# Kernel tuning notes

Measured on AMD Instinct MI355X. Metric: run time of the kernel, lower is better.

## Reference

```python
import jax, jax.numpy as jnp
import numpy as np

N_REC = 12288  # 12 * nside^2, nside=32


def _mlp(x, w1, b1, w2, b2):
    # two-layer MLP with SiLU, as in GraphCast-style edge embedders
    return jnp.dot(jax.nn.silu(jnp.dot(x, w1) + b1), w2) + b2


def setup_inputs() -> dict:
    key = jax.random.key(0)
    ks = jax.random.split(key, 12)
    B, E, D_X, D_EDGE = 2, 393216, 128, 4
    EDGE_IN, EDGE_OUT, LIN_OUT = D_EDGE + D_X, 256, 256

    def glorot(k, shape):
        fan = shape[0] + shape[1]
        return jax.random.normal(k, shape, jnp.float32) * jnp.sqrt(2.0 / fan)

    return {
        "x": jax.random.normal(ks[0], (B, E, D_X), jnp.float32),
        "edge_attr": jax.random.normal(ks[1], (E, D_EDGE), jnp.float32),
        "edge_index": jax.random.randint(ks[2], (2, E), 0, N_REC, jnp.int64),
        "w1e": glorot(ks[3], (EDGE_IN, EDGE_OUT)),
        "b1e": jnp.zeros((EDGE_OUT,), jnp.float32),
        "w2e": glorot(ks[4], (EDGE_OUT, EDGE_OUT)),
        "b2e": jnp.zeros((EDGE_OUT,), jnp.float32),
        "w1f": glorot(ks[5], (EDGE_OUT, LIN_OUT)),
        "b1f": jnp.zeros((LIN_OUT,), jnp.float32),
        "w2f": glorot(ks[6], (LIN_OUT, LIN_OUT)),
        "b2f": jnp.zeros((LIN_OUT,), jnp.float32),
    }


def reference(x, edge_attr, edge_index, w1e, b1e, w2e, b2e, w1f, b1f, w2f, b2f):
    B = x.shape[0]
    # broadcast edge_attr over batch and concat with per-edge grid features
    ea = jnp.broadcast_to(edge_attr[None], (B,) + edge_attr.shape)  # [B,E,d_edge]
    v_g_prime = jnp.concatenate([ea, x], axis=-1)                    # [B,E,edge_in]
    v_g = _mlp(v_g_prime, w1e, b1e, w2e, b2e)                        # [B,E,edge_out]
    # scatter-sum edges into receiver nodes (edge_index[1]) along dim 1
    recv = edge_index[1]
    v_m_sum = jnp.zeros((B, N_REC, v_g.shape[-1]), v_g.dtype).at[:, recv].add(v_g)
    return _mlp(v_m_sum, w1f, b1f, w2f, b2f)                         # [B,N_REC,lin_out]
```

## Files before the change

### kernel.cpp

```cpp
#include <hip/hip_runtime.h>
#include <hip/hip_bf16.h>

#define E_EDGES 393216
#define NRECV   12288
#define DX      128
#define BATCH   2

typedef short bf16x8 __attribute__((ext_vector_type(8)));
typedef float f32x4  __attribute__((ext_vector_type(4)));

__device__ __forceinline__ unsigned short f2bf(float f) {
  union { float f; unsigned u; } v; v.f = f;
  unsigned r = v.u + 0x7FFFu + ((v.u >> 16) & 1u);
  return (unsigned short)(r >> 16);
}

__device__ __forceinline__ unsigned pk2(float a, float b) {
  __hip_bfloat162 h = __float22bfloat162_rn(make_float2(a, b));
  union { __hip_bfloat162 h; unsigned u; } c; c.h = h;
  return c.u;
}

__device__ __forceinline__ float silu_f(float v) {
  return v / (1.0f + __expf(-v));
}

__global__ __launch_bounds__(256) void zero_kernel(float4* __restrict__ p, int n4) {
  int i = blockIdx.x * 256 + threadIdx.x;
  int stride = gridDim.x * 256;
  float4 z = make_float4(0.f, 0.f, 0.f, 0.f);
  for (; i < n4; i += stride) p[i] = z;
}

__global__ void swz_kernel(const float* __restrict__ W,
                           unsigned short* __restrict__ out, int K, int N) {
  int t = blockIdx.x * 256 + threadIdx.x;
  if (t >= K * N) return;
  int j = t & 7;
  int l = (t >> 3) & 63;
  int rest = t >> 9;
  int nfr = N >> 4;
  int nf = rest % nfr;
  int ks = rest / nfr;
  int k = ks * 32 + (l >> 4) * 8 + j;
  int n = nf * 16 + (l & 15);
  out[t] = f2bf(W[k * N + n]);
}

__global__ void swz_w1e_kernel(const float* __restrict__ W, const float* __restrict__ bias,
                               unsigned short* __restrict__ out) {
  int t = blockIdx.x * 256 + threadIdx.x;
  int j = t & 7;
  int l = (t >> 3) & 63;
  int rest = t >> 9;
  int nf = rest & 15;
  int ks = rest >> 4;
  int k = ks * 32 + (l >> 4) * 8 + j;
  int n = nf * 16 + (l & 15);
  float v = (k < 132) ? W[k * 256 + n] : (k == 132 ? bias[n] : 0.0f);
  out[t] = f2bf(v);
}

__global__ void hist_kernel(const int* __restrict__ recv, int* __restrict__ cnt) {
  int e = blockIdx.x * 256 + threadIdx.x;
  if (e < E_EDGES) atomicAdd(&cnt[recv[e]], 1);
}

__global__ __launch_bounds__(256) void scan_kernel(const int* __restrict__ cnt,
                                                   int* __restrict__ head) {
  __shared__ int ts[256];
  const int t = threadIdx.x;
  const int base = t * 48;
  int s = 0;
#pragma unroll
  for (int i = 0; i < 48; ++i) s += cnt[base + i];
  ts[t] = s;
  __syncthreads();
  for (int d = 1; d < 256; d <<= 1) {
    int v = (t >= d) ? ts[t - d] : 0;
    __syncthreads();
    ts[t] += v;
    __syncthreads();
  }
  int run = (t == 0) ? 0 : ts[t - 1];
  for (int i = 0; i < 48; ++i) { head[base + i] = run; run += cnt[base + i]; }
}

__global__ void scatter_kernel(const int* __restrict__ recv, int* __restrict__ head,
                               int* __restrict__ perm) {
  int e = blockIdx.x * 256 + threadIdx.x;
  if (e < E_EDGES) {
    int pos = atomicAdd(&head[recv[e]], 1);
    perm[pos] = e;
  }
}

__global__ __launch_bounds__(256, 4) void edge_kernel(
    const float* __restrict__ x, const float* __restrict__ edge_attr,
    const int* __restrict__ recv, const int* __restrict__ perm,
    const unsigned short* __restrict__ w1sw, float* __restrict__ s) {
  __shared__ __align__(16) char hsT[256 * 144];
  __shared__ __align__(16) char indT[16 * 144];
  __shared__ unsigned int seg32[16];
  __shared__ int seg_recv[64];
  __shared__ int ev[64];
  __shared__ int rs[64];
  char* As = hsT;

  const int tid = threadIdx.x;
  const int l  = tid & 63;
  const int w  = tid >> 6;
  const int lo = l & 15, hi = l >> 4;
  const int p0 = blockIdx.x * 64;
  const int b  = blockIdx.y;

  if (tid < 64) {
    int e = perm[p0 + tid];
    ev[tid] = e;
    rs[tid] = recv[e];
  }
  for (int idx = tid; idx < 960; idx += 256) {
    int r = idx / 15, k2 = idx - r * 15;
    int byte0 = 264 + 8 * k2;
    uint2 vz = make_uint2(k2 == 0 ? 0x00003F80u : 0u, 0u);
    *(uint2*)(As + r * 384 + (byte0 ^ ((r & 7) << 4))) = vz;
  }
  __syncthreads();

  {
    const int r = tid >> 2, q = tid & 3;
    const int e = ev[r];
    const int rx = (r & 7) << 4;
    const float4* xr = (const float4*)(x + ((size_t)b * E_EDGES + e) * DX);
#pragma unroll
    for (int i = 0; i < 8; ++i) {
      int t = i * 4 + q;
      float4 v = xr[t];
      int byte0 = 8 + 8 * t;
      *(uint2*)(As + r * 384 + (byte0 ^ rx)) = make_uint2(pk2(v.x, v.y), pk2(v.z, v.w));
    }
  }
  const int flag = (l == 63) || (rs[l + 1] != rs[l]);
  const unsigned long long segmask = __ballot(flag);
  const int nseg = __popcll(segmask);
  if (tid < 64) {
    float4 ea = *(const float4*)(edge_attr + (size_t)ev[tid] * 4);
    *(uint2*)(As + tid * 384 + ((tid & 7) << 4)) =
        make_uint2(pk2(ea.x, ea.y), pk2(ea.z, ea.w));
    int sid = __popcll(segmask & ((1ull << tid) - 1ull));
    ((unsigned char*)seg32)[tid] = (unsigned char)sid;
    if (flag) seg_recv[sid] = rs[tid];
  }
  __syncthreads();

  {
    int m = tid & 15, k4 = tid >> 4;
    unsigned four = seg32[k4];
    unsigned um = (unsigned)m;
    unsigned e0 = ((four & 255u) == um) ? 0x3F80u : 0u;
    unsigned e1 = (((four >> 8) & 255u) == um) ? 0x3F80u : 0u;
    unsigned e2 = (((four >> 16) & 255u) == um) ? 0x3F80u : 0u;
    unsigned e3 = ((four >> 24) == um) ? 0x3F80u : 0u;
    *(uint2*)(indT + m * 144 + k4 * 8) = make_uint2(e0 | (e1 << 16), e2 | (e3 << 16));
  }

  f32x4 acc[4][4] = {};
  const int axor = (lo & 7) << 4;
#pragma unroll
  for (int kk = 0; kk < 5; ++kk) {
    bf16x8 a[4], bb[4];
#pragma unroll
    for (int mf = 0; mf < 4; ++mf)
      a[mf] = *(const bf16x8*)(As + (mf * 16 + lo) * 384 + ((kk * 64 + hi * 16) ^ axor));
#pragma unroll
    for (int nf = 0; nf < 4; ++nf)
      bb[nf] = *(const bf16x8*)&w1sw[(size_t)(((kk * 16) + (w * 4 + nf)) * 64 + l) * 8];
#pragma unroll
    for (int mf = 0; mf < 4; ++mf)
#pragma unroll
      for (int nf = 0; nf < 4; ++nf)
        acc[mf][nf] = __builtin_amdgcn_mfma_f32_16x16x32_bf16(a[mf], bb[nf], acc[mf][nf], 0, 0, 0);
  }
  __syncthreads();

#pragma unroll
  for (int mf = 0; mf < 4; ++mf) {
#pragma unroll
    for (int nf = 0; nf < 4; ++nf) {
      const int col = w * 64 + nf * 16 + lo;
      float v0 = silu_f(acc[mf][nf][0]);
      float v1 = silu_f(acc[mf][nf][1]);
      float v2 = silu_f(acc[mf][nf][2]);
      float v3 = silu_f(acc[mf][nf][3]);
      *(uint2*)(hsT + col * 144 + (mf * 16 + hi * 4) * 2) =
          make_uint2(pk2(v0, v1), pk2(v2, v3));
    }
  }
  __syncthreads();

  float* sb = s + (size_t)b * NRECV * 256;
  for (int p = 0;;) {
    f32x4 accS[4] = {};
#pragma unroll
    for (int kk = 0; kk < 2; ++kk) {
      bf16x8 a = *(const bf16x8*)(indT + lo * 144 + kk * 64 + hi * 16);
#pragma unroll
      for (int nf = 0; nf < 4; ++nf) {
        bf16x8 bb = *(const bf16x8*)(hsT + (w * 64 + nf * 16 + lo) * 144 + kk * 64 + hi * 16);
        accS[nf] = __builtin_amdgcn_mfma_f32_16x16x32_bf16(a, bb, accS[nf], 0, 0, 0);
      }
    }
#pragma unroll
    for (int j = 0; j < 4; ++j) {
      int sidx = p * 16 + hi * 4 + j;
      if (sidx < nseg) {
        int rcv = seg_recv[sidx];
#pragma unroll
        for (int nf = 0; nf < 4; ++nf)
          atomicAdd(sb + (size_t)rcv * 256 + w * 64 + nf * 16 + lo, accS[nf][j]);
      }
    }
    ++p;
    if (p * 16 >= nseg) break;
    __syncthreads();
    {
      int m = tid & 15, k4 = tid >> 4;
      unsigned four = seg32[k4];
      unsigned um = (unsigned)(m + p * 16);
      unsigned e0 = ((four & 255u) == um) ? 0x3F80u : 0u;
      unsigned e1 = (((four >> 8) & 255u) == um) ? 0x3F80u : 0u;
      unsigned e2 = (((four >> 16) & 255u) == um) ? 0x3F80u : 0u;
      unsigned e3 = ((four >> 24) == um) ? 0x3F80u : 0u;
      *(uint2*)(indT + m * 144 + k4 * 8) = make_uint2(e0 | (e1 << 16), e2 | (e3 << 16));
    }
    __syncthreads();
  }
}

__device__ __forceinline__ void gemm64(const unsigned short* Ns,
                                       const unsigned short* __restrict__ Bsw,
                                       int w, int l, f32x4 acc[4][4]) {
  const int lo = l & 15, hi = l >> 4;
#pragma unroll
  for (int kk = 0; kk < 8; ++kk) {
    bf16x8 a[4], bb[4];
#pragma unroll
    for (int mf = 0; mf < 4; ++mf)
      a[mf] = *(const bf16x8*)&Ns[(mf * 16 + lo) * 264 + kk * 32 + hi * 8];
#pragma unroll
    for (int nf = 0; nf < 4; ++nf)
      bb[nf] = *(const bf16x8*)&Bsw[(size_t)(((kk * 16) + (w * 4 + nf)) * 64 + l) * 8];
#pragma unroll
    for (int mf = 0; mf < 4; ++mf)
#pragma unroll
      for (int nf = 0; nf < 4; ++nf)
        acc[mf][nf] = __builtin_amdgcn_mfma_f32_16x16x32_bf16(a[mf], bb[nf], acc[mf][nf], 0, 0, 0);
  }
}

__global__ __launch_bounds__(256) void node_kernel(
    const float* __restrict__ s, const int* __restrict__ cnt,
    const unsigned short* __restrict__ w2esw, const float* __restrict__ b2e,
    const unsigned short* __restrict__ w1fsw, const float* __restrict__ b1f,
    const unsigned short* __restrict__ w2fsw, const float* __restrict__ b2f,
    float* __restrict__ out) {
  __shared__ unsigned short Ns[64 * 264];
  __shared__ int   cntl[64];
  __shared__ float bias1[256], bias2[256], bias3[256];

  const int tid = threadIdx.x;
  const int l  = tid & 63;
  const int w  = tid >> 6;
  const int lo = l & 15, hi = l >> 4;
  const int r0 = blockIdx.x * 64;
  const int b  = blockIdx.y;

  const float4* sb = (const float4*)(s + ((size_t)b * NRECV + r0) * 256);
#pragma unroll
  for (int i = 0; i < 16; ++i) {
    int f = i * 256 + tid;
    float4 v = sb[f];
    int g = f * 4;
    int row = g >> 8, col = g & 255;
    *(uint2*)&Ns[row * 264 + col] = make_uint2(pk2(v.x, v.y), pk2(v.z, v.w));
  }
  if (tid < 64) cntl[tid] = cnt[r0 + tid];
  bias1[tid] = b2e[tid];
  bias2[tid] = b1f[tid];
  bias3[tid] = b2f[tid];
  __syncthreads();

  {
    f32x4 acc[4][4] = {};
    gemm64(Ns, w2esw, w, l, acc);
    __syncthreads();
#pragma unroll
    for (int mf = 0; mf < 4; ++mf)
#pragma unroll
      for (int nf = 0; nf < 4; ++nf) {
        const int col = w * 64 + nf * 16 + lo;
#pragma unroll
        for (int j = 0; j < 4; ++j) {
          const int row = mf * 16 + hi * 4 + j;
          float v = acc[mf][nf][j] + (float)cntl[row] * bias1[col];
          Ns[row * 264 + col] = f2bf(v);
        }
      }
    __syncthreads();
  }
  {
    f32x4 acc[4][4] = {};
    gemm64(Ns, w1fsw, w, l, acc);
    __syncthreads();
#pragma unroll
    for (int mf = 0; mf < 4; ++mf)
#pragma unroll
      for (int nf = 0; nf < 4; ++nf) {
        const int col = w * 64 + nf * 16 + lo;
#pragma unroll
        for (int j = 0; j < 4; ++j) {
          const int row = mf * 16 + hi * 4 + j;
          float v = silu_f(acc[mf][nf][j] + bias2[col]);
          Ns[row * 264 + col] = f2bf(v);
        }
      }
    __syncthreads();
  }
  {
    f32x4 acc[4][4] = {};
    gemm64(Ns, w2fsw, w, l, acc);
#pragma unroll
    for (int mf = 0; mf < 4; ++mf)
#pragma unroll
      for (int nf = 0; nf < 4; ++nf) {
        const int col = w * 64 + nf * 16 + lo;
#pragma unroll
        for (int j = 0; j < 4; ++j) {
          const int row = mf * 16 + hi * 4 + j;
          out[((size_t)b * NRECV + r0 + row) * 256 + col] = acc[mf][nf][j] + bias3[col];
        }
      }
  }
}

extern "C" void kernel_launch(void* const* d_in, const int* in_sizes, int n_in,
                              void* d_out, int out_size, void* d_ws, size_t ws_size,
                              hipStream_t stream) {
  const float* x         = (const float*)d_in[0];
  const float* edge_attr = (const float*)d_in[1];
  const int*   edge_idx  = (const int*)d_in[2];
  const float* w1e       = (const float*)d_in[3];
  const float* b1e       = (const float*)d_in[4];
  const float* w2e       = (const float*)d_in[5];
  const float* b2e       = (const float*)d_in[6];
  const float* w1f       = (const float*)d_in[7];
  const float* b1f       = (const float*)d_in[8];
  const float* w2f       = (const float*)d_in[9];
  const float* b2f       = (const float*)d_in[10];
  float* out = (float*)d_out;

  char* ws = (char*)d_ws;
  float*          sbuf  = (float*)(ws + 0);
  int*            cnt   = (int*)(ws + 25165824);
  int*            head  = (int*)(ws + 25214976);
  int*            perm  = (int*)(ws + 25264128);
  unsigned short* w1sw  = (unsigned short*)(ws + 26836992);
  unsigned short* w2esw = (unsigned short*)(ws + 26918912);
  unsigned short* w1fsw = (unsigned short*)(ws + 27049984);
  unsigned short* w2fsw = (unsigned short*)(ws + 27181056);

  zero_kernel<<<2048, 256, 0, stream>>>((float4*)ws, 1575936);

  swz_w1e_kernel<<<160, 256, 0, stream>>>(w1e, b1e, w1sw);
  swz_kernel<<<(256 * 256) / 256, 256, 0, stream>>>(w2e, w2esw, 256, 256);
  swz_kernel<<<(256 * 256) / 256, 256, 0, stream>>>(w1f, w1fsw, 256, 256);
  swz_kernel<<<(256 * 256) / 256, 256, 0, stream>>>(w2f, w2fsw, 256, 256);

  const int* recv = edge_idx + E_EDGES;
  hist_kernel<<<E_EDGES / 256, 256, 0, stream>>>(recv, cnt);
  scan_kernel<<<1, 256, 0, stream>>>(cnt, head);
  scatter_kernel<<<E_EDGES / 256, 256, 0, stream>>>(recv, head, perm);

  dim3 eg(E_EDGES / 64, BATCH);
  edge_kernel<<<eg, 256, 0, stream>>>(x, edge_attr, recv, perm, w1sw, sbuf);

  dim3 ng(NRECV / 64, BATCH);
  node_kernel<<<ng, 256, 0, stream>>>(sbuf, cnt, w2esw, b2e, w1fsw, b1f, w2fsw, b2f, out);
}
```

Baseline: 278.6 us.

## Keep SiLU hidden tile in registers via shuffles and merge weight swizzle kernels

The edge kernel now passes the SiLU activations to the segment-sum MFMA through wavefront shuffles instead of a transposed LDS buffer. It builds the indicator operand directly in registers, which removes several barriers and shrinks shared memory from about 39KB to about 25KB. x and edge_attr loads are issued into registers before the LDS setup so they overlap it, and SiLU uses the exp2 and rcp intrinsics. The four weight-swizzle launches are merged into one kernel, at the cost of extra register pressure from holding the packed activations.

```diff
diff --git a/kernel.cpp b/kernel.cpp
--- a/kernel.cpp
+++ b/kernel.cpp
@@ -22,7 +22,8 @@
 }
 
 __device__ __forceinline__ float silu_f(float v) {
-  return v / (1.0f + __expf(-v));
+  float e = __builtin_amdgcn_exp2f(v * -1.44269504089f);
+  return v * __builtin_amdgcn_rcpf(1.0f + e);
 }
 
 __global__ __launch_bounds__(256) void zero_kernel(float4* __restrict__ p, int n4) {
@@ -32,33 +33,33 @@
   for (; i < n4; i += stride) p[i] = z;
 }
 
-__global__ void swz_kernel(const float* __restrict__ W,
-                           unsigned short* __restrict__ out, int K, int N) {
-  int t = blockIdx.x * 256 + threadIdx.x;
-  if (t >= K * N) return;
-  int j = t & 7;
-  int l = (t >> 3) & 63;
-  int rest = t >> 9;
-  int nfr = N >> 4;
-  int nf = rest % nfr;
-  int ks = rest / nfr;
-  int k = ks * 32 + (l >> 4) * 8 + j;
-  int n = nf * 16 + (l & 15);
-  out[t] = f2bf(W[k * N + n]);
-}
-
-__global__ void swz_w1e_kernel(const float* __restrict__ W, const float* __restrict__ bias,
-                               unsigned short* __restrict__ out) {
-  int t = blockIdx.x * 256 + threadIdx.x;
-  int j = t & 7;
-  int l = (t >> 3) & 63;
-  int rest = t >> 9;
-  int nf = rest & 15;
-  int ks = rest >> 4;
-  int k = ks * 32 + (l >> 4) * 8 + j;
-  int n = nf * 16 + (l & 15);
-  float v = (k < 132) ? W[k * 256 + n] : (k == 132 ? bias[n] : 0.0f);
-  out[t] = f2bf(v);
+__global__ __launch_bounds__(256) void swz_all_kernel(
+    const float* __restrict__ w1e, const float* __restrict__ b1e,
+    const float* __restrict__ w2e, const float* __restrict__ w1f,
+    const float* __restrict__ w2f,
+    unsigned short* __restrict__ w1sw, unsigned short* __restrict__ w2esw,
+    unsigned short* __restrict__ w1fsw, unsigned short* __restrict__ w2fsw) {
+  int blk = blockIdx.x;
+  if (blk < 160) {
+    int t = blk * 256 + threadIdx.x;
+    int j = t & 7, l = (t >> 3) & 63, rest = t >> 9;
+    int nf = rest & 15, ks = rest >> 4;
+    int k = ks * 32 + (l >> 4) * 8 + j;
+    int n = nf * 16 + (l & 15);
+    float v = (k < 132) ? w1e[k * 256 + n] : (k == 132 ? b1e[n] : 0.0f);
+    w1sw[t] = f2bf(v);
+  } else {
+    int g = blk - 160;
+    int which = g >> 8;
+    int t = (g & 255) * 256 + threadIdx.x;
+    const float* W = (which == 0) ? w2e : (which == 1) ? w1f : w2f;
+    unsigned short* O = (which == 0) ? w2esw : (which == 1) ? w1fsw : w2fsw;
+    int j = t & 7, l = (t >> 3) & 63, rest = t >> 9;
+    int nf = rest & 15, ks = rest >> 4;
+    int k = ks * 32 + (l >> 4) * 8 + j;
+    int n = nf * 16 + (l & 15);
+    O[t] = f2bf(W[k * 256 + n]);
+  }
 }
 
 __global__ void hist_kernel(const int* __restrict__ recv, int* __restrict__ cnt) {
@@ -99,13 +100,10 @@
     const float* __restrict__ x, const float* __restrict__ edge_attr,
     const int* __restrict__ recv, const int* __restrict__ perm,
     const unsigned short* __restrict__ w1sw, float* __restrict__ s) {
-  __shared__ __align__(16) char hsT[256 * 144];
-  __shared__ __align__(16) char indT[16 * 144];
-  __shared__ unsigned int seg32[16];
+  __shared__ __align__(16) char As[64 * 384];
+  __shared__ int rs[64];
   __shared__ int seg_recv[64];
-  __shared__ int ev[64];
-  __shared__ int rs[64];
-  char* As = hsT;
+  __shared__ unsigned seg32[16];
 
   const int tid = threadIdx.x;
   const int l  = tid & 63;
@@ -114,55 +112,51 @@
   const int p0 = blockIdx.x * 64;
   const int b  = blockIdx.y;
 
+  const int r = tid >> 2, q = tid & 3;
+  const int er = perm[p0 + r];
+  const float4* xr = (const float4*)(x + ((size_t)b * E_EDGES + er) * DX);
+  float4 xv[8];
+#pragma unroll
+  for (int i = 0; i < 8; ++i) xv[i] = xr[i * 4 + q];
+
+  float4 ea;
   if (tid < 64) {
-    int e = perm[p0 + tid];
-    ev[tid] = e;
-    rs[tid] = recv[e];
-  }
+    int e1 = perm[p0 + tid];
+    rs[tid] = recv[e1];
+    ea = *(const float4*)(edge_attr + (size_t)e1 * 4);
+  }
+
   for (int idx = tid; idx < 960; idx += 256) {
-    int r = idx / 15, k2 = idx - r * 15;
+    int rr = idx / 15, k2 = idx - rr * 15;
     int byte0 = 264 + 8 * k2;
     uint2 vz = make_uint2(k2 == 0 ? 0x00003F80u : 0u, 0u);
-    *(uint2*)(As + r * 384 + (byte0 ^ ((r & 7) << 4))) = vz;
-  }
-  __syncthreads();
+    *(uint2*)(As + rr * 384 + (byte0 ^ ((rr & 7) << 4))) = vz;
+  }
 
   {
-    const int r = tid >> 2, q = tid & 3;
-    const int e = ev[r];
     const int rx = (r & 7) << 4;
-    const float4* xr = (const float4*)(x + ((size_t)b * E_EDGES + e) * DX);
 #pragma unroll
     for (int i = 0; i < 8; ++i) {
       int t = i * 4 + q;
-      float4 v = xr[t];
       int byte0 = 8 + 8 * t;
-      *(uint2*)(As + r * 384 + (byte0 ^ rx)) = make_uint2(pk2(v.x, v.y), pk2(v.z, v.w));
+      *(uint2*)(As + r * 384 + (byte0 ^ rx)) =
+          make_uint2(pk2(xv[i].x, xv[i].y), pk2(xv[i].z, xv[i].w));
     }
   }
+  if (tid < 64) {
+    *(uint2*)(As + tid * 384 + ((tid & 7) << 4)) =
+        make_uint2(pk2(ea.x, ea.y), pk2(ea.z, ea.w));
+  }
+  __syncthreads();
+
   const int flag = (l == 63) || (rs[l + 1] != rs[l]);
   const unsigned long long segmask = __ballot(flag);
   const int nseg = __popcll(segmask);
   if (tid < 64) {
-    float4 ea = *(const float4*)(edge_attr + (size_t)ev[tid] * 4);
-    *(uint2*)(As + tid * 384 + ((tid & 7) << 4)) =
-        make_uint2(pk2(ea.x, ea.y), pk2(ea.z, ea.w));
     int sid = __popcll(segmask & ((1ull << tid) - 1ull));
     ((unsigned char*)seg32)[tid] = (unsigned char)sid;
     if (flag) seg_recv[sid] = rs[tid];
   }
-  __syncthreads();
-
-  {
-    int m = tid & 15, k4 = tid >> 4;
-    unsigned four = seg32[k4];
-    unsigned um = (unsigned)m;
-    unsigned e0 = ((four & 255u) == um) ? 0x3F80u : 0u;
-    unsigned e1 = (((four >> 8) & 255u) == um) ? 0x3F80u : 0u;
-    unsigned e2 = (((four >> 16) & 255u) == um) ? 0x3F80u : 0u;
-    unsigned e3 = ((four >> 24) == um) ? 0x3F80u : 0u;
-    *(uint2*)(indT + m * 144 + k4 * 8) = make_uint2(e0 | (e1 << 16), e2 | (e3 << 16));
-  }
 
   f32x4 acc[4][4] = {};
   const int axor = (lo & 7) << 4;
@@ -183,33 +177,59 @@
   }
   __syncthreads();
 
-#pragma unroll
-  for (int mf = 0; mf < 4; ++mf) {
+  unsigned pkd[4][4][2];
+#pragma unroll
+  for (int mf = 0; mf < 4; ++mf)
 #pragma unroll
     for (int nf = 0; nf < 4; ++nf) {
-      const int col = w * 64 + nf * 16 + lo;
       float v0 = silu_f(acc[mf][nf][0]);
       float v1 = silu_f(acc[mf][nf][1]);
       float v2 = silu_f(acc[mf][nf][2]);
       float v3 = silu_f(acc[mf][nf][3]);
-      *(uint2*)(hsT + col * 144 + (mf * 16 + hi * 4) * 2) =
-          make_uint2(pk2(v0, v1), pk2(v2, v3));
+      pkd[mf][nf][0] = pk2(v0, v1);
+      pkd[mf][nf][1] = pk2(v2, v3);
     }
-  }
-  __syncthreads();
+
+  unsigned hbw[2][4][4];
+#pragma unroll
+  for (int kk = 0; kk < 2; ++kk)
+#pragma unroll
+    for (int nf = 0; nf < 4; ++nf)
+#pragma unroll
+      for (int t = 0; t < 4; ++t) {
+        int src = ((hi & 1) * 2 + (t >> 1)) * 16 + lo;
+        int a0 = __shfl((int)pkd[2 * kk][nf][t & 1], src, 64);
+        int a1 = __shfl((int)pkd[2 * kk + 1][nf][t & 1], src, 64);
+        hbw[kk][nf][t] = (hi & 2) ? (unsigned)a1 : (unsigned)a0;
+      }
 
   float* sb = s + (size_t)b * NRECV * 256;
-  for (int p = 0;;) {
+  for (int p = 0; p * 16 < nseg; ++p) {
+    union { unsigned u[4]; bf16x8 v; } ia[2];
+#pragma unroll
+    for (int kk = 0; kk < 2; ++kk) {
+      unsigned d0 = seg32[kk * 8 + hi * 2];
+      unsigned d1 = seg32[kk * 8 + hi * 2 + 1];
+      unsigned tgt = (unsigned)(lo + p * 16);
+      ia[kk].u[0] = (((d0 & 255u) == tgt) ? 0x3F80u : 0u) |
+                    ((((d0 >> 8) & 255u) == tgt) ? 0x3F800000u : 0u);
+      ia[kk].u[1] = ((((d0 >> 16) & 255u) == tgt) ? 0x3F80u : 0u) |
+                    (((d0 >> 24) == tgt) ? 0x3F800000u : 0u);
+      ia[kk].u[2] = (((d1 & 255u) == tgt) ? 0x3F80u : 0u) |
+                    ((((d1 >> 8) & 255u) == tgt) ? 0x3F800000u : 0u);
+      ia[kk].u[3] = ((((d1 >> 16) & 255u) == tgt) ? 0x3F80u : 0u) |
+                    (((d1 >> 24) == tgt) ? 0x3F800000u : 0u);
+    }
     f32x4 accS[4] = {};
 #pragma unroll
-    for (int kk = 0; kk < 2; ++kk) {
-      bf16x8 a = *(const bf16x8*)(indT + lo * 144 + kk * 64 + hi * 16);
+    for (int kk = 0; kk < 2; ++kk)
 #pragma unroll
       for (int nf = 0; nf < 4; ++nf) {
-        bf16x8 bb = *(const bf16x8*)(hsT + (w * 64 + nf * 16 + lo) * 144 + kk * 64 + hi * 16);
-        accS[nf] = __builtin_amdgcn_mfma_f32_16x16x32_bf16(a, bb, accS[nf], 0, 0, 0);
-      }
-    }
+        union { unsigned u[4]; bf16x8 v; } hb;
+        hb.u[0] = hbw[kk][nf][0]; hb.u[1] = hbw[kk][nf][1];
+        hb.u[2] = hbw[kk][nf][2]; hb.u[3] = hbw[kk][nf][3];
+        accS[nf] = __builtin_amdgcn_mfma_f32_16x16x32_bf16(ia[kk].v, hb.v, accS[nf], 0, 0, 0);
+      }
 #pragma unroll
     for (int j = 0; j < 4; ++j) {
       int sidx = p * 16 + hi * 4 + j;
@@ -220,20 +240,6 @@
           atomicAdd(sb + (size_t)rcv * 256 + w * 64 + nf * 16 + lo, accS[nf][j]);
       }
     }
-    ++p;
-    if (p * 16 >= nseg) break;
-    __syncthreads();
-    {
-      int m = tid & 15, k4 = tid >> 4;
-      unsigned four = seg32[k4];
-      unsigned um = (unsigned)(m + p * 16);
-      unsigned e0 = ((four & 255u) == um) ? 0x3F80u : 0u;
-      unsigned e1 = (((four >> 8) & 255u) == um) ? 0x3F80u : 0u;
-      unsigned e2 = (((four >> 16) & 255u) == um) ? 0x3F80u : 0u;
-      unsigned e3 = ((four >> 24) == um) ? 0x3F80u : 0u;
-      *(uint2*)(indT + m * 144 + k4 * 8) = make_uint2(e0 | (e1 << 16), e2 | (e3 << 16));
-    }
-    __syncthreads();
   }
 }
 
@@ -371,10 +377,8 @@
 
   zero_kernel<<<2048, 256, 0, stream>>>((float4*)ws, 1575936);
 
-  swz_w1e_kernel<<<160, 256, 0, stream>>>(w1e, b1e, w1sw);
-  swz_kernel<<<(256 * 256) / 256, 256, 0, stream>>>(w2e, w2esw, 256, 256);
-  swz_kernel<<<(256 * 256) / 256, 256, 0, stream>>>(w1f, w1fsw, 256, 256);
-  swz_kernel<<<(256 * 256) / 256, 256, 0, stream>>>(w2f, w2fsw, 256, 256);
+  swz_all_kernel<<<928, 256, 0, stream>>>(w1e, b1e, w2e, w1f, w2f,
+                                          w1sw, w2esw, w1fsw, w2fsw);
 
   const int* recv = edge_idx + E_EDGES;
   hist_kernel<<<E_EDGES / 256, 256, 0, stream>>>(recv, cnt);
```

Result: faster. 250.3 us (-10.2%).
